# Kernel tuning notes

Hardware: AMD Instinct MI355X
Metric: run time of the kernel (lower is better)

Reference implementation:

```python
import jax, jax.numpy as jnp
import numpy as np

B, T, D, N = 4, 2048, 1024, 16

def setup_inputs() -> dict:
    key = jax.random.key(0)
    ks = jax.random.split(key, 6)
    scale = 0.02
    return {
        'x': jax.random.normal(ks[0], (B, T, D), dtype=jnp.float32),
        'Wd': jax.random.normal(ks[1], (D, D), dtype=jnp.float32) * (1.0 / np.sqrt(D)),
        'bd': jnp.zeros((D,), dtype=jnp.float32),
        'a_log': jax.random.normal(ks[2], (D, N), dtype=jnp.float32) * scale,
        'b_param': jax.random.normal(ks[3], (D, N), dtype=jnp.float32) * scale,
        'Wo': jax.random.normal(ks[4], (D, D), dtype=jnp.float32) * (1.0 / np.sqrt(D)),
        'bo': jnp.zeros((D,), dtype=jnp.float32),
    }

def reference(x, Wd, bd, a_log, b_param, Wo, bo):
    # delta: [B,T,D]
    delta = jax.nn.softplus(jnp.einsum('btd,ed->bte', x, Wd) + bd)
    a_pos = jax.nn.softplus(a_log) + 1e-4  # [D,N]

    def step(state, inputs):
        x_t, delta_t = inputs  # [B,D], [B,D]
        dt = delta_t[..., None]                      # [B,D,1]
        a_bar = jnp.exp(-dt * a_pos)                 # [B,D,N]
        state = a_bar * state + (dt * b_param) * x_t[..., None]
        return state, state.sum(axis=-1)             # y_t: [B,D]

    init = jnp.zeros((B, D, N), dtype=x.dtype)
    xs = (jnp.swapaxes(x, 0, 1), jnp.swapaxes(delta, 0, 1))  # [T,B,D]
    _, y = jax.lax.scan(step, init, xs)              # y: [T,B,D]
    y = jnp.swapaxes(y, 0, 1)                        # [B,T,D]
    return jnp.einsum('btd,ed->bte', y, Wo) + bo
```

## Files before the change

### kernel.cpp

```cpp
#include <hip/hip_runtime.h>
#include <hip/hip_bf16.h>

#define B_ 4
#define T_ 2048
#define D_ 1024
#define N_ 16
#define TCH 32
#define NCH 64

typedef __attribute__((ext_vector_type(4))) float f32x4;
typedef __attribute__((ext_vector_type(8))) short short8;
typedef unsigned int u32;
typedef unsigned short u16;

#if defined(__has_builtin)
#if __has_builtin(__builtin_amdgcn_exp2f)
#define EXP2(x) __builtin_amdgcn_exp2f(x)
#else
#define EXP2(x) exp2f(x)
#endif
#else
#define EXP2(x) exp2f(x)
#endif

__device__ __forceinline__ float softplus_f(float v) {
    return v > 20.f ? v : log1pf(__expf(v));
}

__device__ __forceinline__ u16 f2bf(float f) {
    u32 u = __float_as_uint(f);
    u32 r = (u + 0x7fffu + ((u >> 16) & 1u)) >> 16;
    return (u16)r;
}

__global__ __launch_bounds__(256) void cvt_f32_bf16(const float* __restrict__ in,
                                                    u16* __restrict__ out, int n4) {
    int i = blockIdx.x * 256 + threadIdx.x;
    if (i >= n4) return;
    float4 v = ((const float4*)in)[i];
    ushort4 o;
    o.x = f2bf(v.x); o.y = f2bf(v.y); o.z = f2bf(v.z); o.w = f2bf(v.w);
    ((ushort4*)out)[i] = o;
}

template <int ACT>
__global__ __launch_bounds__(512, 8) void gemm_bt(const u16* __restrict__ A,
                                                  const u16* __restrict__ Bw,
                                                  const float* __restrict__ bias,
                                                  float* __restrict__ C,
                                                  int M, int N, int K) {
    __shared__ __align__(16) u16 sA[64 * 64];
    __shared__ __align__(16) u16 sB[128 * 64];
    const int tid = threadIdx.x;
    const int wid = tid >> 6;
    const int lane = tid & 63;

    const int wg = blockIdx.x;
    const int xcd = wg & 7;
    const int jj = wg >> 3;
    const int npm8 = (M / 64) >> 3;
    const int bx = xcd * npm8 + (jj % npm8);
    const int by = jj / npm8;
    const int m0 = bx * 64;
    const int n0 = by * 128;
    const int wm = wid >> 2;
    const int wn = wid & 3;

    const int lrow = lane >> 3;
    const int slot = lane & 7;
    const int ksw = (slot ^ lrow) << 3;

    const u16* aP  = A  + (size_t)(m0 + wid * 8 + lrow) * K + ksw;
    const u16* bP0 = Bw + (size_t)(n0 + wid * 8 + lrow) * K + ksw;
    const u16* bP1 = Bw + (size_t)(n0 + (wid + 8) * 8 + lrow) * K + ksw;
    const int dsA  = wid * 1024 + lrow * 128 + slot * 16;
    const int dsB0 = dsA;
    const int dsB1 = (wid + 8) * 1024 + lrow * 128 + slot * 16;

    short8 ra, rb0, rb1;
    f32x4 acc[2][2] = {};
    const int nt = K / 64;
    const int fr = lane & 15;
    const int g = lane >> 4;
    const int xorv = (fr & 7) << 4;

    ra  = *(const short8*)(aP);
    rb0 = *(const short8*)(bP0);
    rb1 = *(const short8*)(bP1);
    *(short8*)((char*)sA + dsA)  = ra;
    *(short8*)((char*)sB + dsB0) = rb0;
    *(short8*)((char*)sB + dsB1) = rb1;
    ra  = *(const short8*)(aP + 64);
    rb0 = *(const short8*)(bP0 + 64);
    rb1 = *(const short8*)(bP1 + 64);
    asm volatile("s_waitcnt lgkmcnt(0)" ::: "memory");
    __builtin_amdgcn_s_barrier();
    asm volatile("" ::: "memory");

    for (int t = 0; t < nt; ++t) {
        #pragma unroll
        for (int kk = 0; kk < 2; ++kk) {
            const int ksb = (kk * 64 + g * 16) ^ xorv;
            short8 af[2], bf[2];
            #pragma unroll
            for (int f = 0; f < 2; ++f)
                af[f] = *(const short8*)((const char*)sA + (wm * 32 + f * 16 + fr) * 128 + ksb);
            #pragma unroll
            for (int f = 0; f < 2; ++f)
                bf[f] = *(const short8*)((const char*)sB + (wn * 32 + f * 16 + fr) * 128 + ksb);
            __builtin_amdgcn_s_setprio(1);
            #pragma unroll
            for (int i = 0; i < 2; ++i)
                #pragma unroll
                for (int j2 = 0; j2 < 2; ++j2)
                    acc[i][j2] = __builtin_amdgcn_mfma_f32_16x16x32_bf16(af[i], bf[j2],
                                                                         acc[i][j2], 0, 0, 0);
            __builtin_amdgcn_s_setprio(0);
        }
        if (t + 1 < nt) {
            asm volatile("s_waitcnt lgkmcnt(0)" ::: "memory");
            __builtin_amdgcn_s_barrier();
            asm volatile("" ::: "memory");
            *(short8*)((char*)sA + dsA)  = ra;
            *(short8*)((char*)sB + dsB0) = rb0;
            *(short8*)((char*)sB + dsB1) = rb1;
            asm volatile("s_waitcnt lgkmcnt(0)" ::: "memory");
            __builtin_amdgcn_s_barrier();
            asm volatile("" ::: "memory");
            if (t + 2 < nt) {
                const int k0 = (t + 2) * 64;
                ra  = *(const short8*)(aP + k0);
                rb0 = *(const short8*)(bP0 + k0);
                rb1 = *(const short8*)(bP1 + k0);
            }
        }
    }

    const int cl = lane & 15;
    const int rg = (lane >> 4) * 4;
    #pragma unroll
    for (int j2 = 0; j2 < 2; ++j2) {
        const int col = n0 + wn * 32 + j2 * 16 + cl;
        const float bv = bias[col];
        #pragma unroll
        for (int i = 0; i < 2; ++i) {
            #pragma unroll
            for (int r = 0; r < 4; ++r) {
                const int rowg = m0 + wm * 32 + i * 16 + rg + r;
                float v = acc[i][j2][r] + bv;
                if (ACT) v = softplus_f(v);
                C[(size_t)rowg * N + col] = v;
            }
        }
    }
}

__global__ __launch_bounds__(256) void scan_p1(const float* __restrict__ delta,
                                               const float* __restrict__ x,
                                               const float* __restrict__ a_log,
                                               float* __restrict__ S,
                                               float* __restrict__ dtsum) {
    const int gid = blockIdx.x * 256 + threadIdx.x;
    const int lane = gid & 63;
    const int w = gid >> 6;
    const int dw = w & 31;
    const int cb = w >> 5;
    const int d = dw * 32 + (lane & 31);
    const int half = lane >> 5;
    const int b = cb & (B_ - 1);
    const int c = cb >> 2;

    float an2[8];
    {
        const float4* a4 = (const float4*)&a_log[d * N_ + half * 8];
        float4 a0 = a4[0], a1 = a4[1];
        an2[0] = (softplus_f(a0.x) + 1e-4f) * 1.44269504f;
        an2[1] = (softplus_f(a0.y) + 1e-4f) * 1.44269504f;
        an2[2] = (softplus_f(a0.z) + 1e-4f) * 1.44269504f;
        an2[3] = (softplus_f(a0.w) + 1e-4f) * 1.44269504f;
        an2[4] = (softplus_f(a1.x) + 1e-4f) * 1.44269504f;
        an2[5] = (softplus_f(a1.y) + 1e-4f) * 1.44269504f;
        an2[6] = (softplus_f(a1.z) + 1e-4f) * 1.44269504f;
        an2[7] = (softplus_f(a1.w) + 1e-4f) * 1.44269504f;
    }

    float s[8];
    #pragma unroll
    for (int n = 0; n < 8; ++n) s[n] = 0.f;
    float dts = 0.f;

    const size_t base = ((size_t)b * T_ + (size_t)c * TCH) * D_ + d;
    for (int i = 0; i < TCH; ++i) {
        const float dt = delta[base + (size_t)i * D_];
        const float xv = x[base + (size_t)i * D_];
        const float dtx = dt * xv;
        dts += dt;
        #pragma unroll
        for (int n = 0; n < 8; ++n) {
            const float ab = EXP2(-dt * an2[n]);
            s[n] = fmaf(ab, s[n], dtx);
        }
    }

    float4* So = (float4*)&S[((size_t)cb * D_ + d) * N_ + half * 8];
    So[0] = make_float4(s[0], s[1], s[2], s[3]);
    So[1] = make_float4(s[4], s[5], s[6], s[7]);
    if (half == 0) dtsum[(size_t)cb * D_ + d] = dts;
}

__global__ __launch_bounds__(256) void scan_p2(const float* __restrict__ S,
                                               const float* __restrict__ dtsum,
                                               const float* __restrict__ a_log,
                                               float* __restrict__ carry_out) {
    const int gid = blockIdx.x * 256 + threadIdx.x;
    const int n = gid & 15;
    const int d = (gid >> 4) & (D_ - 1);
    const int b = gid >> 14;
    const float an2 = (softplus_f(a_log[d * N_ + n]) + 1e-4f) * 1.44269504f;
    float carry = 0.f;
    for (int c = 0; c < NCH; ++c) {
        const size_t cb = (size_t)c * B_ + b;
        const size_t idx = (cb * D_ + d) * N_ + n;
        carry_out[idx] = carry;
        const float dts = dtsum[cb * D_ + d];
        const float P = EXP2(-dts * an2);
        carry = fmaf(P, carry, S[idx]);
    }
}

__global__ __launch_bounds__(256) void scan_p3(const float* __restrict__ delta,
                                               const float* __restrict__ x,
                                               const float* __restrict__ a_log,
                                               const float* __restrict__ b_param,
                                               const float* __restrict__ carry_in,
                                               u16* __restrict__ y) {
    const int gid = blockIdx.x * 256 + threadIdx.x;
    const int lane = gid & 63;
    const int w = gid >> 6;
    const int dw = w & 31;
    const int cb = w >> 5;
    const int d = dw * 32 + (lane & 31);
    const int half = lane >> 5;
    const int b = cb & (B_ - 1);
    const int c = cb >> 2;

    float an2[8], bp[8];
    {
        const float4* a4 = (const float4*)&a_log[d * N_ + half * 8];
        const float4* b4 = (const float4*)&b_param[d * N_ + half * 8];
        float4 a0 = a4[0], a1 = a4[1];
        float4 v0 = b4[0], v1 = b4[1];
        an2[0] = (softplus_f(a0.x) + 1e-4f) * 1.44269504f;
        an2[1] = (softplus_f(a0.y) + 1e-4f) * 1.44269504f;
        an2[2] = (softplus_f(a0.z) + 1e-4f) * 1.44269504f;
        an2[3] = (softplus_f(a0.w) + 1e-4f) * 1.44269504f;
        an2[4] = (softplus_f(a1.x) + 1e-4f) * 1.44269504f;
        an2[5] = (softplus_f(a1.y) + 1e-4f) * 1.44269504f;
        an2[6] = (softplus_f(a1.z) + 1e-4f) * 1.44269504f;
        an2[7] = (softplus_f(a1.w) + 1e-4f) * 1.44269504f;
        bp[0] = v0.x; bp[1] = v0.y; bp[2] = v0.z; bp[3] = v0.w;
        bp[4] = v1.x; bp[5] = v1.y; bp[6] = v1.z; bp[7] = v1.w;
    }

    float s[8];
    {
        const float4* ci = (const float4*)&carry_in[((size_t)cb * D_ + d) * N_ + half * 8];
        float4 c0 = ci[0], c1 = ci[1];
        s[0] = c0.x; s[1] = c0.y; s[2] = c0.z; s[3] = c0.w;
        s[4] = c1.x; s[5] = c1.y; s[6] = c1.z; s[7] = c1.w;
    }

    const size_t base = ((size_t)b * T_ + (size_t)c * TCH) * D_ + d;
    for (int i = 0; i < TCH; ++i) {
        const float dt = delta[base + (size_t)i * D_];
        const float xv = x[base + (size_t)i * D_];
        const float dtx = dt * xv;
        float acc = 0.f;
        #pragma unroll
        for (int n = 0; n < 8; ++n) {
            const float ab = EXP2(-dt * an2[n]);
            s[n] = fmaf(ab, s[n], dtx);
            acc = fmaf(bp[n], s[n], acc);
        }
        const float tot = acc + __shfl_xor(acc, 32);
        if (half == 0) y[base + (size_t)i * D_] = f2bf(tot);
    }
}

extern "C" void kernel_launch(void* const* d_in, const int* in_sizes, int n_in,
                              void* d_out, int out_size, void* d_ws, size_t ws_size,
                              hipStream_t stream) {
    const float* x      = (const float*)d_in[0];
    const float* Wd     = (const float*)d_in[1];
    const float* bd     = (const float*)d_in[2];
    const float* a_log  = (const float*)d_in[3];
    const float* b_par  = (const float*)d_in[4];
    const float* Wo     = (const float*)d_in[5];
    const float* bo     = (const float*)d_in[6];
    float* out = (float*)d_out;

    char* ws = (char*)d_ws;
    u16*   xbf     = (u16*)(ws);
    float* carry   = (float*)(ws);
    float* S       = (float*)(ws + 16777216);
    u16*   ybf     = (u16*)(ws + 16777216);
    float* delta   = (float*)(ws + 33554432);
    u16*   wdbf    = (u16*)(ws + 67108864);
    u16*   wobf    = (u16*)(ws + 69206016);
    float* dtsum   = (float*)(ws + 71303168);
    (void)in_sizes; (void)n_in; (void)out_size; (void)ws_size;

    const int M = B_ * T_;

    cvt_f32_bf16<<<(M * D_ / 4 + 255) / 256, 256, 0, stream>>>(x, xbf, M * D_ / 4);
    cvt_f32_bf16<<<(D_ * D_ / 4 + 255) / 256, 256, 0, stream>>>(Wd, wdbf, D_ * D_ / 4);
    cvt_f32_bf16<<<(D_ * D_ / 4 + 255) / 256, 256, 0, stream>>>(Wo, wobf, D_ * D_ / 4);

    gemm_bt<1><<<(M / 64) * (D_ / 128), 512, 0, stream>>>(xbf, wdbf, bd, delta, M, D_, D_);

    scan_p1<<<NCH * B_ * D_ * 2 / 256, 256, 0, stream>>>(delta, x, a_log, S, dtsum);
    scan_p2<<<B_ * D_ * N_ / 256, 256, 0, stream>>>(S, dtsum, a_log, carry);
    scan_p3<<<NCH * B_ * D_ * 2 / 256, 256, 0, stream>>>(delta, x, a_log, b_par, carry, ybf);

    gemm_bt<0><<<(M / 64) * (D_ / 128), 512, 0, stream>>>(ybf, wobf, bo, out, M, D_, D_);
}
```

Measured before the change: 173.7 us.

## Use direct global-to-LDS loads with double-buffered shared tiles in GEMM

The GEMM now loads tiles with global_load_lds straight into shared memory instead of staging them through registers. Shared memory is double-buffered so the next K tile is fetched while the current one feeds the MFMAs, and there is one barrier per iteration instead of two. Problem dimensions become compile-time constants so the K loop can be fully unrolled. Shared memory per block doubles and the occupancy hint drops from 8 to 6, and the per-lane swizzled destination addresses that the direct-to-LDS path needs may not match the layout the reads expect.

```diff
diff --git a/kernel.cpp b/kernel.cpp
--- a/kernel.cpp
+++ b/kernel.cpp
@@ -7,6 +7,10 @@
 #define N_ 16
 #define TCH 32
 #define NCH 64
+
+#define GM 8192
+#define GK 1024
+#define GN 1024
 
 typedef __attribute__((ext_vector_type(4))) float f32x4;
 typedef __attribute__((ext_vector_type(8))) short short8;
@@ -43,14 +47,18 @@
     ((ushort4*)out)[i] = o;
 }
 
+__device__ __forceinline__ void gload_lds16(const void* g, void* l) {
+    __builtin_amdgcn_global_load_lds((const __attribute__((address_space(1))) u32*)g,
+                                     (__attribute__((address_space(3))) u32*)l, 16, 0, 0);
+}
+
 template <int ACT>
-__global__ __launch_bounds__(512, 8) void gemm_bt(const u16* __restrict__ A,
+__global__ __launch_bounds__(512, 6) void gemm_bt(const u16* __restrict__ A,
                                                   const u16* __restrict__ Bw,
                                                   const float* __restrict__ bias,
-                                                  float* __restrict__ C,
-                                                  int M, int N, int K) {
-    __shared__ __align__(16) u16 sA[64 * 64];
-    __shared__ __align__(16) u16 sB[128 * 64];
+                                                  float* __restrict__ C) {
+    __shared__ __align__(16) u16 sA[2][64 * 64];
+    __shared__ __align__(16) u16 sB[2][128 * 64];
     const int tid = threadIdx.x;
     const int wid = tid >> 6;
     const int lane = tid & 63;
@@ -58,9 +66,8 @@
     const int wg = blockIdx.x;
     const int xcd = wg & 7;
     const int jj = wg >> 3;
-    const int npm8 = (M / 64) >> 3;
-    const int bx = xcd * npm8 + (jj % npm8);
-    const int by = jj / npm8;
+    const int bx = xcd * 16 + (jj & 15);
+    const int by = jj >> 4;
     const int m0 = bx * 64;
     const int n0 = by * 128;
     const int wm = wid >> 2;
@@ -70,44 +77,42 @@
     const int slot = lane & 7;
     const int ksw = (slot ^ lrow) << 3;
 
-    const u16* aP  = A  + (size_t)(m0 + wid * 8 + lrow) * K + ksw;
-    const u16* bP0 = Bw + (size_t)(n0 + wid * 8 + lrow) * K + ksw;
-    const u16* bP1 = Bw + (size_t)(n0 + (wid + 8) * 8 + lrow) * K + ksw;
-    const int dsA  = wid * 1024 + lrow * 128 + slot * 16;
-    const int dsB0 = dsA;
-    const int dsB1 = (wid + 8) * 1024 + lrow * 128 + slot * 16;
-
-    short8 ra, rb0, rb1;
+    const u16* aP  = A  + (size_t)(m0 + wid * 8 + lrow) * GK + ksw;
+    const u16* bP0 = Bw + (size_t)(n0 + wid * 8 + lrow) * GK + ksw;
+    const u16* bP1 = Bw + (size_t)(n0 + (wid + 8) * 8 + lrow) * GK + ksw;
+    const int ldsA  = wid * 1024;
+    const int ldsB1 = (wid + 8) * 1024;
+
     f32x4 acc[2][2] = {};
-    const int nt = K / 64;
     const int fr = lane & 15;
     const int g = lane >> 4;
     const int xorv = (fr & 7) << 4;
 
-    ra  = *(const short8*)(aP);
-    rb0 = *(const short8*)(bP0);
-    rb1 = *(const short8*)(bP1);
-    *(short8*)((char*)sA + dsA)  = ra;
-    *(short8*)((char*)sB + dsB0) = rb0;
-    *(short8*)((char*)sB + dsB1) = rb1;
-    ra  = *(const short8*)(aP + 64);
-    rb0 = *(const short8*)(bP0 + 64);
-    rb1 = *(const short8*)(bP1 + 64);
-    asm volatile("s_waitcnt lgkmcnt(0)" ::: "memory");
-    __builtin_amdgcn_s_barrier();
-    asm volatile("" ::: "memory");
-
-    for (int t = 0; t < nt; ++t) {
+    gload_lds16(aP,  (char*)sA[0] + ldsA);
+    gload_lds16(bP0, (char*)sB[0] + ldsA);
+    gload_lds16(bP1, (char*)sB[0] + ldsB1);
+
+    #pragma unroll
+    for (int t = 0; t < GK / 64; ++t) {
+        __syncthreads();
+        if (t + 1 < GK / 64) {
+            const int nb = (t + 1) & 1;
+            gload_lds16(aP  + (t + 1) * 64, (char*)sA[nb] + ldsA);
+            gload_lds16(bP0 + (t + 1) * 64, (char*)sB[nb] + ldsA);
+            gload_lds16(bP1 + (t + 1) * 64, (char*)sB[nb] + ldsB1);
+        }
+        const char* bA = (const char*)sA[t & 1];
+        const char* bB = (const char*)sB[t & 1];
         #pragma unroll
         for (int kk = 0; kk < 2; ++kk) {
             const int ksb = (kk * 64 + g * 16) ^ xorv;
             short8 af[2], bf[2];
             #pragma unroll
             for (int f = 0; f < 2; ++f)
-                af[f] = *(const short8*)((const char*)sA + (wm * 32 + f * 16 + fr) * 128 + ksb);
+                af[f] = *(const short8*)(bA + (wm * 32 + f * 16 + fr) * 128 + ksb);
             #pragma unroll
             for (int f = 0; f < 2; ++f)
-                bf[f] = *(const short8*)((const char*)sB + (wn * 32 + f * 16 + fr) * 128 + ksb);
+                bf[f] = *(const short8*)(bB + (wn * 32 + f * 16 + fr) * 128 + ksb);
             __builtin_amdgcn_s_setprio(1);
             #pragma unroll
             for (int i = 0; i < 2; ++i)
@@ -116,23 +121,6 @@
                     acc[i][j2] = __builtin_amdgcn_mfma_f32_16x16x32_bf16(af[i], bf[j2],
                                                                          acc[i][j2], 0, 0, 0);
             __builtin_amdgcn_s_setprio(0);
-        }
-        if (t + 1 < nt) {
-            asm volatile("s_waitcnt lgkmcnt(0)" ::: "memory");
-            __builtin_amdgcn_s_barrier();
-            asm volatile("" ::: "memory");
-            *(short8*)((char*)sA + dsA)  = ra;
-            *(short8*)((char*)sB + dsB0) = rb0;
-            *(short8*)((char*)sB + dsB1) = rb1;
-            asm volatile("s_waitcnt lgkmcnt(0)" ::: "memory");
-            __builtin_amdgcn_s_barrier();
-            asm volatile("" ::: "memory");
-            if (t + 2 < nt) {
-                const int k0 = (t + 2) * 64;
-                ra  = *(const short8*)(aP + k0);
-                rb0 = *(const short8*)(bP0 + k0);
-                rb1 = *(const short8*)(bP1 + k0);
-            }
         }
     }
 
@@ -149,7 +137,7 @@
                 const int rowg = m0 + wm * 32 + i * 16 + rg + r;
                 float v = acc[i][j2][r] + bv;
                 if (ACT) v = softplus_f(v);
-                C[(size_t)rowg * N + col] = v;
+                C[(size_t)rowg * GN + col] = v;
             }
         }
     }
@@ -316,11 +304,11 @@
     cvt_f32_bf16<<<(D_ * D_ / 4 + 255) / 256, 256, 0, stream>>>(Wd, wdbf, D_ * D_ / 4);
     cvt_f32_bf16<<<(D_ * D_ / 4 + 255) / 256, 256, 0, stream>>>(Wo, wobf, D_ * D_ / 4);
 
-    gemm_bt<1><<<(M / 64) * (D_ / 128), 512, 0, stream>>>(xbf, wdbf, bd, delta, M, D_, D_);
+    gemm_bt<1><<<(GM / 64) * (GN / 128), 512, 0, stream>>>(xbf, wdbf, bd, delta);
 
     scan_p1<<<NCH * B_ * D_ * 2 / 256, 256, 0, stream>>>(delta, x, a_log, S, dtsum);
     scan_p2<<<B_ * D_ * N_ / 256, 256, 0, stream>>>(S, dtsum, a_log, carry);
     scan_p3<<<NCH * B_ * D_ * 2 / 256, 256, 0, stream>>>(delta, x, a_log, b_par, carry, ybf);
 
-    gemm_bt<0><<<(M / 64) * (D_ / 128), 512, 0, stream>>>(ybf, wobf, bo, out, M, D_, D_);
-}
+    gemm_bt<0><<<(GM / 64) * (GN / 128), 512, 0, stream>>>(ybf, wobf, bo, out);
+}
```

Result: no change. 176.1 us (+1.4%).
